# Kernel tuning notes

Measured on AMD Instinct MI355X. Metric: run time of the kernel, lower is better.

The kernel has to match this reference:

```python
import jax, jax.numpy as jnp
from jax import lax
import numpy as np

D_MODEL, N_STATES, N_GROUPS, K_CONV = 1024, 16, 8, 4
BATCH, LENGTH = 2, 2048


def setup_inputs() -> dict:
    key = jax.random.key(0)
    ks = jax.random.split(key, 8)
    x = jax.random.normal(ks[0], (BATCH, LENGTH, D_MODEL), dtype=jnp.float32)
    in_proj_w = jax.random.normal(ks[1], (2 * D_MODEL, D_MODEL), dtype=jnp.float32) * 0.02
    in_proj_b = jnp.zeros((2 * D_MODEL,), dtype=jnp.float32)
    delta_proj_w = jax.random.uniform(ks[2], (D_MODEL, D_MODEL), dtype=jnp.float32, minval=0.001, maxval=0.1)
    a_log = jnp.log(jnp.tile(jnp.arange(1, N_STATES + 1, dtype=jnp.float32), (D_MODEL, 1)))
    b_proj_w = jax.random.normal(ks[3], (N_GROUPS * N_STATES, D_MODEL), dtype=jnp.float32) * 1e-4
    b_proj_b = jnp.zeros((N_GROUPS * N_STATES,), dtype=jnp.float32)
    c_param = jax.random.normal(ks[4], (D_MODEL, N_STATES), dtype=jnp.float32) * 0.02
    # depthwise conv (groups = d_model): kernel [D, 1, K]
    conv_w = jax.random.normal(ks[5], (D_MODEL, 1, K_CONV), dtype=jnp.float32) * (1.0 / np.sqrt(K_CONV))
    conv_b = jnp.zeros((D_MODEL,), dtype=jnp.float32)
    return {"x": x, "in_proj_w": in_proj_w, "in_proj_b": in_proj_b,
            "delta_proj_w": delta_proj_w, "a_log": a_log,
            "b_proj_w": b_proj_w, "b_proj_b": b_proj_b, "c_param": c_param,
            "conv_w": conv_w, "conv_b": conv_b}


def _causal_conv(u, conv_w, conv_b):
    # u: [B, L, D] -> depthwise causal conv along L
    D = u.shape[-1]
    K = conv_w.shape[-1]
    uc = jnp.transpose(u, (0, 2, 1))  # [B, D, L]
    uc = lax.conv_general_dilated(uc, conv_w, window_strides=(1,),
                                  padding=[(K - 1, 0)], feature_group_count=D,
                                  dimension_numbers=("NCH", "OIH", "NCH"))
    uc = uc + conv_b[None, :, None]
    return jnp.transpose(uc, (0, 2, 1))  # [B, L, D]


def _selective_scan(delta, A, Bmat, c_param, u):
    # delta,u: [B,L,D]; A: [D,N]; Bmat: [B,L,G,N]; c_param: [D,N]
    Bsz, L, D = delta.shape
    N = A.shape[1]
    G = Bmat.shape[2]
    Bexp = jnp.repeat(Bmat, D // G, axis=2)            # [B,L,D,N]
    dA = jnp.exp(delta[..., None] * A)                  # [B,L,D,N]
    dBu = (delta * u)[..., None] * Bexp                 # [B,L,D,N]

    def step(h, xs):
        da, dbu = xs
        h = da * h + dbu                                # [B,D,N]
        y = jnp.einsum("bdn,dn->bd", h, c_param)
        return h, y

    h0 = jnp.zeros((Bsz, D, N), dtype=delta.dtype)
    _, ys = lax.scan(step, h0, (jnp.moveaxis(dA, 1, 0), jnp.moveaxis(dBu, 1, 0)))
    return jnp.moveaxis(ys, 0, 1)                       # [B,L,D]


def reference(x, in_proj_w, in_proj_b, delta_proj_w, a_log, b_proj_w, b_proj_b, c_param, conv_w, conv_b):
    Bsz, L, _ = x.shape
    N = a_log.shape[1]
    G = b_proj_w.shape[0] // N
    xp = x @ in_proj_w.T + in_proj_b                    # [B,L,2D]
    u, v = jnp.split(xp, 2, axis=-1)
    delta = jax.nn.softplus(u @ delta_proj_w.T)         # [B,L,D]
    A = -jnp.exp(a_log)                                 # [D,N]
    Bmat = (u @ b_proj_w.T + b_proj_b).reshape(Bsz, L, G, N)
    u_conv = jax.nn.silu(_causal_conv(u, conv_w, conv_b))
    y = _selective_scan(delta, A, Bmat, c_param, u_conv)
    return y * jax.nn.silu(v)
```

## Files before the change

kernel.cpp:

```cpp
#include <hip/hip_runtime.h>
#include <math.h>

#define LTOT 2048
#define MROWS 4096
#define CHK 64
#define NCH (LTOT / CHK)
#define SPAD 20

typedef short bf16x8 __attribute__((ext_vector_type(8)));
typedef float f32x4  __attribute__((ext_vector_type(4)));
typedef float f32x16 __attribute__((ext_vector_type(16)));

__device__ __forceinline__ unsigned short bf16_rne(float f) {
  unsigned u = __float_as_uint(f);
  u += 0x7FFF + ((u >> 16) & 1);
  return (unsigned short)(u >> 16);
}
__device__ __forceinline__ float bf16_to_f(unsigned short h) {
  return __uint_as_float(((unsigned)h) << 16);
}
__device__ __forceinline__ float softplus_f(float x) {
  return (x > 15.f) ? x : log1pf(expf(x));
}
__device__ __forceinline__ float silu_f(float x) {
  return x / (1.f + expf(-x));
}

__global__ void k_cvt_all(const float* __restrict__ x, const float* __restrict__ w1,
                          const float* __restrict__ dw, const float* __restrict__ bw,
                          unsigned short* __restrict__ xh, unsigned short* __restrict__ xl,
                          unsigned short* __restrict__ wfh, unsigned short* __restrict__ wfl,
                          unsigned short* __restrict__ wdbAh, unsigned short* __restrict__ wdbAl) {
  const int blk = blockIdx.x;
  const float* src; unsigned short *h, *l; int i;
  if (blk < 4096)      { src = x;  h = xh;  l = xl;  i = blk * 256 + threadIdx.x; }
  else if (blk < 6144) { src = w1; h = wfh; l = wfl; i = (blk - 4096) * 256 + threadIdx.x; }
  else if (blk < 7168) { src = dw; h = wdbAh; l = wdbAl; i = (blk - 6144) * 256 + threadIdx.x; }
  else                 { src = bw; h = wdbAh + (size_t)1024*1024; l = wdbAl + (size_t)1024*1024;
                         i = (blk - 7168) * 256 + threadIdx.x; }
  const float4 v = ((const float4*)src)[i];
  ushort4 hh, ll;
  hh.x = bf16_rne(v.x); ll.x = bf16_rne(v.x - bf16_to_f(hh.x));
  hh.y = bf16_rne(v.y); ll.y = bf16_rne(v.y - bf16_to_f(hh.y));
  hh.z = bf16_rne(v.z); ll.z = bf16_rne(v.z - bf16_to_f(hh.z));
  hh.w = bf16_rne(v.w); ll.w = bf16_rne(v.w - bf16_to_f(hh.w));
  ((ushort4*)h)[i] = hh;
  ((ushort4*)l)[i] = ll;
}

__global__ __launch_bounds__(256) void k_cvt_t(const float* __restrict__ w1,
    unsigned short* __restrict__ th, unsigned short* __restrict__ tl) {
  __shared__ float ts[64][65];
  const int t = threadIdx.x;
  const int j0 = blockIdx.y * 64, k0 = blockIdx.x * 64;
  const int r = t >> 4, c4 = (t & 15) * 4;
  #pragma unroll
  for (int p = 0; p < 4; ++p) {
    const int row = p * 16 + r;
    const float4 v = *(const float4*)&w1[(size_t)(j0 + row) * 1024 + k0 + c4];
    ts[row][c4] = v.x; ts[row][c4+1] = v.y; ts[row][c4+2] = v.z; ts[row][c4+3] = v.w;
  }
  __syncthreads();
  #pragma unroll
  for (int p = 0; p < 4; ++p) {
    const int rk = p * 16 + r;
    ushort4 hh, ll;
    float f;
    f = ts[c4+0][rk]; hh.x = bf16_rne(f); ll.x = bf16_rne(f - bf16_to_f(hh.x));
    f = ts[c4+1][rk]; hh.y = bf16_rne(f); ll.y = bf16_rne(f - bf16_to_f(hh.y));
    f = ts[c4+2][rk]; hh.z = bf16_rne(f); ll.z = bf16_rne(f - bf16_to_f(hh.z));
    f = ts[c4+3][rk]; hh.w = bf16_rne(f); ll.w = bf16_rne(f - bf16_to_f(hh.w));
    *(ushort4*)&th[(size_t)(k0 + rk) * 1024 + j0 + c4] = hh;
    *(ushort4*)&tl[(size_t)(k0 + rk) * 1024 + j0 + c4] = ll;
  }
}

__global__ void k_bias(const float* __restrict__ b1, const float* __restrict__ dw,
                       const float* __restrict__ bw, const float* __restrict__ bb,
                       float* __restrict__ bfull) {
  const int t = threadIdx.x;
  const int j = blockIdx.x * 16 + (t >> 4);
  const int lane16 = t & 15;
  const float* W = (j < 1024) ? (dw + (size_t)j * 1024) : (bw + (size_t)(j - 1024) * 1024);
  float s = 0.f;
  for (int i = 0; i < 64; ++i) {
    const int k = lane16 + i * 16;
    s = fmaf(b1[k], W[k], s);
  }
  s += __shfl_xor(s, 8, 16);
  s += __shfl_xor(s, 4, 16);
  s += __shfl_xor(s, 2, 16);
  s += __shfl_xor(s, 1, 16);
  if (lane16 == 0) bfull[j] = s + ((j >= 1024) ? bb[j - 1024] : 0.f);
}

__global__ __launch_bounds__(256) void k_wcomp(
    const unsigned short* __restrict__ Ah_g, const unsigned short* __restrict__ Al_g,
    const unsigned short* __restrict__ Bh_g, const unsigned short* __restrict__ Bl_g,
    unsigned short* __restrict__ outh, unsigned short* __restrict__ outl) {
  __shared__ __align__(16) unsigned short LAh[64*32];
  __shared__ __align__(16) unsigned short LAl[64*32];
  __shared__ __align__(16) unsigned short LBh[64*32];
  __shared__ __align__(16) unsigned short LBl[64*32];
  const int t = threadIdx.x;
  const int wave = t >> 6, lane = t & 63;
  const int m0 = blockIdx.y * 64, n0 = blockIdx.x * 64;
  const int wr = wave >> 1, wc = wave & 1;
  const int l32 = lane & 31, hi = lane >> 5;
  const int srow = lane >> 2, scol = (lane & 3) * 8;

  f32x16 acc;
  #pragma unroll
  for (int q = 0; q < 16; ++q) acc[q] = 0.f;

  auto stage = [&](const unsigned short* g, unsigned short* lds, int rbase, int k0) {
    const unsigned short* gp = g + (size_t)(rbase + wave * 16 + srow) * 1024 + k0 + scol;
    unsigned short* lp = lds + (wave * 16) * 32;
    __builtin_amdgcn_global_load_lds((const __attribute__((address_space(1))) void*)gp,
                                     (__attribute__((address_space(3))) void*)lp, 16, 0, 0);
  };

  for (int k0 = 0; k0 < 1024; k0 += 32) {
    __syncthreads();
    stage(Ah_g, LAh, m0, k0);
    stage(Al_g, LAl, m0, k0);
    stage(Bh_g, LBh, n0, k0);
    stage(Bl_g, LBl, n0, k0);
    __syncthreads();
    #pragma unroll
    for (int kh = 0; kh < 2; ++kh) {
      const int ai = (wr * 32 + l32) * 32 + kh * 16 + hi * 8;
      const int bi = (wc * 32 + l32) * 32 + kh * 16 + hi * 8;
      bf16x8 a_h = *(const bf16x8*)&LAh[ai];
      bf16x8 a_l = *(const bf16x8*)&LAl[ai];
      bf16x8 b_h = *(const bf16x8*)&LBh[bi];
      bf16x8 b_l = *(const bf16x8*)&LBl[bi];
      acc = __builtin_amdgcn_mfma_f32_32x32x16_bf16(a_h, b_h, acc, 0, 0, 0);
      acc = __builtin_amdgcn_mfma_f32_32x32x16_bf16(a_h, b_l, acc, 0, 0, 0);
      acc = __builtin_amdgcn_mfma_f32_32x32x16_bf16(a_l, b_h, acc, 0, 0, 0);
    }
  }

  #pragma unroll
  for (int reg = 0; reg < 16; ++reg) {
    const int i = m0 + wr * 32 + (reg & 3) + 8 * (reg >> 2) + 4 * hi;
    const int k = n0 + wc * 32 + l32;
    const float f = acc[reg];
    const unsigned short hh = bf16_rne(f);
    const unsigned short ll = bf16_rne(f - bf16_to_f(hh));
    outh[(size_t)i * 1024 + k] = hh;
    outl[(size_t)i * 1024 + k] = ll;
  }
}

__global__ __launch_bounds__(256) void k_main(
    const unsigned short* __restrict__ xh, const unsigned short* __restrict__ xl,
    const unsigned short* __restrict__ wfh, const unsigned short* __restrict__ wfl,
    const float* __restrict__ b1, const float* __restrict__ bfull,
    float* __restrict__ u_, float* __restrict__ v_,
    float* __restrict__ delta, float* __restrict__ Bm) {
  __shared__ __align__(16) unsigned short LAh[128*32];
  __shared__ __align__(16) unsigned short LAl[128*32];
  __shared__ __align__(16) unsigned short LBh[128*32];
  __shared__ __align__(16) unsigned short LBl[128*32];
  const int t = threadIdx.x;
  const int wave = t >> 6, lane = t & 63;
  const int flat = blockIdx.x;
  const int wg = (flat & 7) * 100 + (flat >> 3);
  const int tn = wg % 25;
  const int m0 = (wg / 25) * 128;
  const int wr = wave >> 1, wc = wave & 1;
  const int ln = lane & 15, kq = lane >> 4;
  const int srow = lane >> 2, scol = (lane & 3) * 8;
  const bool full = (tn >= 16);

  f32x4 acc[4][4];
  #pragma unroll
  for (int i = 0; i < 4; ++i)
    #pragma unroll
    for (int j = 0; j < 4; ++j) acc[i][j] = (f32x4){0.f, 0.f, 0.f, 0.f};

  const unsigned short* pAh = xh + (size_t)m0 * 1024;
  const unsigned short* pAl = xl + (size_t)m0 * 1024;
  const unsigned short* pBh = wfh + (size_t)(tn * 128) * 1024;
  const unsigned short* pBl = wfl + (size_t)(tn * 128) * 1024;

  auto stage = [&](const unsigned short* g, unsigned short* lds, int k0) {
    #pragma unroll
    for (int r = 0; r < 2; ++r) {
      const unsigned short* gp = g + (size_t)(r * 64 + wave * 16 + srow) * 1024 + k0 + scol;
      unsigned short* lp = lds + (r * 64 + wave * 16) * 32;
      __builtin_amdgcn_global_load_lds((const __attribute__((address_space(1))) void*)gp,
                                       (__attribute__((address_space(3))) void*)lp, 16, 0, 0);
    }
  };

  for (int k0 = 0; k0 < 1024; k0 += 32) {
    __syncthreads();
    stage(pAh, LAh, k0);
    stage(pBh, LBh, k0);
    if (full) { stage(pAl, LAl, k0); stage(pBl, LBl, k0); }
    __syncthreads();

    if (full) {
      bf16x8 ah[4], al[4], bh[4], bl[4];
      #pragma unroll
      for (int i = 0; i < 4; ++i) {
        const int ar = (wr * 64 + i * 16 + ln) * 32 + kq * 8;
        const int br = (wc * 64 + i * 16 + ln) * 32 + kq * 8;
        ah[i] = *(const bf16x8*)&LAh[ar];
        al[i] = *(const bf16x8*)&LAl[ar];
        bh[i] = *(const bf16x8*)&LBh[br];
        bl[i] = *(const bf16x8*)&LBl[br];
      }
      #pragma unroll
      for (int i = 0; i < 4; ++i)
        #pragma unroll
        for (int j = 0; j < 4; ++j) {
          acc[i][j] = __builtin_amdgcn_mfma_f32_16x16x32_bf16(ah[i], bh[j], acc[i][j], 0, 0, 0);
          acc[i][j] = __builtin_amdgcn_mfma_f32_16x16x32_bf16(ah[i], bl[j], acc[i][j], 0, 0, 0);
          acc[i][j] = __builtin_amdgcn_mfma_f32_16x16x32_bf16(al[i], bh[j], acc[i][j], 0, 0, 0);
        }
    } else {
      bf16x8 ah[4], bh[4];
      #pragma unroll
      for (int i = 0; i < 4; ++i) {
        const int ar = (wr * 64 + i * 16 + ln) * 32 + kq * 8;
        const int br = (wc * 64 + i * 16 + ln) * 32 + kq * 8;
        ah[i] = *(const bf16x8*)&LAh[ar];
        bh[i] = *(const bf16x8*)&LBh[br];
      }
      #pragma unroll
      for (int i = 0; i < 4; ++i)
        #pragma unroll
        for (int j = 0; j < 4; ++j)
          acc[i][j] = __builtin_amdgcn_mfma_f32_16x16x32_bf16(ah[i], bh[j], acc[i][j], 0, 0, 0);
    }
  }

  #pragma unroll
  for (int nj = 0; nj < 4; ++nj) {
    const int colg = tn * 128 + wc * 64 + nj * 16 + ln;
    const float bv = (tn < 16) ? b1[colg] : bfull[colg - 2048];
    #pragma unroll
    for (int mi = 0; mi < 4; ++mi) {
      const int row = m0 + wr * 64 + mi * 16 + kq * 4;
      #pragma unroll
      for (int j = 0; j < 4; ++j) {
        const float val = acc[mi][nj][j] + bv;
        if (tn < 8)       u_[(size_t)(row + j) * 1024 + colg] = val;
        else if (tn < 16) v_[(size_t)(row + j) * 1024 + colg - 1024] = val;
        else if (tn < 24) delta[(size_t)(row + j) * 1024 + colg - 2048] = softplus_f(val);
        else              Bm[(size_t)(row + j) * 128 + colg - 3072] = val;
      }
    }
  }
}

__global__ __launch_bounds__(256) void k_scanA(
    const float* __restrict__ delta, const float* __restrict__ u_,
    const float* __restrict__ Bm, const float* __restrict__ a_log,
    const float* __restrict__ cw, const float* __restrict__ cb,
    float* __restrict__ hend, float* __restrict__ Pp)
{
  __shared__ float sru[68][SPAD];
  __shared__ float sd[CHK][SPAD];
  __shared__ float sb[CHK][SPAD];
  __shared__ float suc[CHK][SPAD];
  const int t = threadIdx.x;
  const int bid = blockIdx.x;
  const int dblk = bid & 63;
  const int ch   = (bid >> 6) & (NCH - 1);
  const int b    = bid >> 11;
  const int d0 = dblk * 16;
  const int g  = dblk >> 3;
  const int l0 = ch * CHK;
  const size_t mb = (size_t)b * LTOT;

  {
    const int lrow = t >> 2;
    const int lc4  = (t & 3) * 4;
    const size_t r = mb + l0 + lrow;
    float4 rd = *(const float4*)&delta[r*1024 + d0 + lc4];
    float4 rb = *(const float4*)&Bm[r*128 + g*16 + lc4];
    *(float4*)&sd[lrow][lc4] = rd;
    *(float4*)&sb[lrow][lc4] = rb;
    const int sl = l0 + lrow - 4;
    float4 ru = (sl >= 0) ? *(const float4*)&u_[(mb + sl)*1024 + d0 + lc4]
                          : (float4){0.f, 0.f, 0.f, 0.f};
    *(float4*)&sru[lrow][lc4] = ru;
    if (t < 16) {
      const int rr2 = 64 + (t >> 2);
      const int sl2 = l0 + rr2 - 4;
      float4 r2 = *(const float4*)&u_[(mb + sl2)*1024 + d0 + (t & 3) * 4];
      *(float4*)&sru[rr2][(t & 3) * 4] = r2;
    }
  }
  __syncthreads();
  {
    const int c = t & 15;
    const int rb4 = (t >> 4) * 4;
    const float4 cwf = *(const float4*)&cw[(d0 + c) * 4];
    const float cbf = cb[d0 + c];
    #pragma unroll
    for (int q = 0; q < 4; ++q) {
      const int l = rb4 + q;
      float a = cbf;
      a = fmaf(sru[l+1][c], cwf.x, a);
      a = fmaf(sru[l+2][c], cwf.y, a);
      a = fmaf(sru[l+3][c], cwf.z, a);
      a = fmaf(sru[l+4][c], cwf.w, a);
      suc[l][c] = silu_f(a);
    }
  }
  __syncthreads();

  const int gi = t >> 4;
  const int n  = t & 15;
  const int d  = d0 + gi;
  const float A2 = -expf(a_log[d*16 + n]) * 1.4426950408889634f;

  float h = 0.f, P = 1.f;
  #pragma unroll 8
  for (int l = 0; l < CHK; ++l) {
    const float dv = sd[l][gi];
    const float uv = suc[l][gi];
    const float bv = sb[l][n];
    const float da = exp2f(dv * A2);
    P *= da;
    h = fmaf(da, h, dv * uv * bv);
  }
  const size_t idx = ((size_t)(b*NCH + ch) * 1024 + d) * 16 + n;
  hend[idx] = h;
  Pp[idx]   = P;
}

__global__ void k_scanB(float* hP, const float* __restrict__ Pp)
{
  const int t = blockIdx.x * 256 + threadIdx.x;
  const int b  = t >> 14;
  const int dn = t & 16383;
  float H = 0.f;
  for (int ch = 0; ch < NCH; ++ch) {
    const size_t idx = ((size_t)(b*NCH + ch) << 14) + dn;
    const float he = hP[idx];
    const float P  = Pp[idx];
    hP[idx] = H;
    H = fmaf(P, H, he);
  }
}

__global__ __launch_bounds__(256) void k_scanC(
    const float* __restrict__ v_, const float* __restrict__ delta,
    const float* __restrict__ u_, const float* __restrict__ Bm,
    const float* __restrict__ a_log, const float* __restrict__ cp,
    const float* __restrict__ cw, const float* __restrict__ cb,
    const float* __restrict__ Hstart, float* __restrict__ out)
{
  __shared__ float sru[68][SPAD];
  __shared__ float sd[CHK][SPAD];
  __shared__ float sb[CHK][SPAD];
  __shared__ float suc[CHK][SPAD];
  __shared__ float sv[CHK][SPAD];
  __shared__ float sy[CHK][SPAD];
  const int t = threadIdx.x;
  const int bid = blockIdx.x;
  const int dblk = bid & 63;
  const int ch   = (bid >> 6) & (NCH - 1);
  const int b    = bid >> 11;
  const int d0 = dblk * 16;
  const int g  = dblk >> 3;
  const int l0 = ch * CHK;
  const size_t mb = (size_t)b * LTOT;

  {
    const int lrow = t >> 2;
    const int lc4  = (t & 3) * 4;
    const size_t r = mb + l0 + lrow;
    float4 rd = *(const float4*)&delta[r*1024 + d0 + lc4];
    float4 rb = *(const float4*)&Bm[r*128 + g*16 + lc4];
    float4 rv = *(const float4*)&v_[r*1024 + d0 + lc4];
    *(float4*)&sd[lrow][lc4] = rd;
    *(float4*)&sb[lrow][lc4] = rb;
    *(float4*)&sv[lrow][lc4] = rv;
    const int sl = l0 + lrow - 4;
    float4 ru = (sl >= 0) ? *(const float4*)&u_[(mb + sl)*1024 + d0 + lc4]
                          : (float4){0.f, 0.f, 0.f, 0.f};
    *(float4*)&sru[lrow][lc4] = ru;
    if (t < 16) {
      const int rr2 = 64 + (t >> 2);
      const int sl2 = l0 + rr2 - 4;
      float4 r2 = *(const float4*)&u_[(mb + sl2)*1024 + d0 + (t & 3) * 4];
      *(float4*)&sru[rr2][(t & 3) * 4] = r2;
    }
  }
  __syncthreads();
  {
    const int c = t & 15;
    const int rb4 = (t >> 4) * 4;
    const float4 cwf = *(const float4*)&cw[(d0 + c) * 4];
    const float cbf = cb[d0 + c];
    #pragma unroll
    for (int q = 0; q < 4; ++q) {
      const int l = rb4 + q;
      float a = cbf;
      a = fmaf(sru[l+1][c], cwf.x, a);
      a = fmaf(sru[l+2][c], cwf.y, a);
      a = fmaf(sru[l+3][c], cwf.z, a);
      a = fmaf(sru[l+4][c], cwf.w, a);
      suc[l][c] = silu_f(a);
    }
  }
  __syncthreads();

  const int gi = t >> 4;
  const int n  = t & 15;
  const int d  = d0 + gi;
  const float A2 = -expf(a_log[d*16 + n]) * 1.4426950408889634f;
  const float cc = cp[d*16 + n];
  float h = Hstart[((size_t)(b*NCH + ch) * 1024 + d) * 16 + n];

  #pragma unroll
  for (int l16 = 0; l16 < CHK; l16 += 16) {
    float p[16];
    #pragma unroll
    for (int j = 0; j < 16; ++j) {
      const int l = l16 + j;
      const float dv = sd[l][gi];
      const float uv = suc[l][gi];
      const float bv = sb[l][n];
      const float da = exp2f(dv * A2);
      h = fmaf(da, h, dv * uv * bv);
      p[j] = h * cc;
    }
    float q8[8];
    #pragma unroll
    for (int j = 0; j < 8; ++j) {
      const float send = (n & 8) ? p[j]     : p[j + 8];
      const float keep = (n & 8) ? p[j + 8] : p[j];
      q8[j] = keep + __shfl_xor(send, 8, 16);
    }
    float q4[4];
    #pragma unroll
    for (int j = 0; j < 4; ++j) {
      const float send = (n & 4) ? q8[j]     : q8[j + 4];
      const float keep = (n & 4) ? q8[j + 4] : q8[j];
      q4[j] = keep + __shfl_xor(send, 4, 16);
    }
    float q2[2];
    #pragma unroll
    for (int j = 0; j < 2; ++j) {
      const float send = (n & 2) ? q4[j]     : q4[j + 2];
      const float keep = (n & 2) ? q4[j + 2] : q4[j];
      q2[j] = keep + __shfl_xor(send, 2, 16);
    }
    {
      const float send = (n & 1) ? q2[0] : q2[1];
      const float keep = (n & 1) ? q2[1] : q2[0];
      sy[l16 + n][gi] = keep + __shfl_xor(send, 1, 16);
    }
  }

  __syncthreads();
  const int rr = t >> 4;
  const int c  = t & 15;
  #pragma unroll
  for (int k = 0; k < 4; ++k) {
    const int r = rr + k * 16;
    const float vv = sv[r][c];
    out[(mb + l0 + r) * 1024 + d0 + c] = sy[r][c] * silu_f(vv);
  }
}

extern "C" void kernel_launch(void* const* d_in, const int* in_sizes, int n_in,
                              void* d_out, int out_size, void* d_ws, size_t ws_size,
                              hipStream_t stream) {
  const float* x    = (const float*)d_in[0];
  const float* w1   = (const float*)d_in[1];
  const float* b1   = (const float*)d_in[2];
  const float* dw   = (const float*)d_in[3];
  const float* alog = (const float*)d_in[4];
  const float* bw   = (const float*)d_in[5];
  const float* bb   = (const float*)d_in[6];
  const float* cp   = (const float*)d_in[7];
  const float* cw   = (const float*)d_in[8];
  const float* cb   = (const float*)d_in[9];
  float* out = (float*)d_out;

  const size_t M4 = (size_t)MROWS * 1024;
  float* u_    = (float*)d_ws;
  float* v_    = u_ + M4;
  float* delta = v_ + M4;
  float* Bm    = delta + M4;
  unsigned short* xh  = (unsigned short*)(Bm + (size_t)MROWS * 128);
  unsigned short* xl  = xh + M4;
  unsigned short* wfh = xl + M4;
  unsigned short* wfl = wfh + (size_t)3200 * 1024;
  float* bfull = (float*)(wfl + (size_t)3200 * 1024);
  unsigned short* wdbAh = (unsigned short*)delta;
  unsigned short* wdbAl = wdbAh + (size_t)1152 * 1024;
  unsigned short* w1th  = wdbAl + (size_t)1152 * 1024;
  unsigned short* w1tl  = w1th + (size_t)1024 * 1024;
  float* hend = (float*)wfh;
  float* Pp   = hend + (size_t)2 * NCH * 1024 * 16;

  k_cvt_all<<<7296, 256, 0, stream>>>(x, w1, dw, bw, xh, xl, wfh, wfl, wdbAh, wdbAl);
  k_cvt_t<<<dim3(16, 16), 256, 0, stream>>>(w1, w1th, w1tl);
  k_bias<<<72, 256, 0, stream>>>(b1, dw, bw, bb, bfull);
  k_wcomp<<<dim3(16, 18), 256, 0, stream>>>(wdbAh, wdbAl, w1th, w1tl,
                                            wfh + (size_t)2048*1024, wfl + (size_t)2048*1024);
  k_main<<<800, 256, 0, stream>>>(xh, xl, wfh, wfl, b1, bfull, u_, v_, delta, Bm);
  k_scanA<<<2 * NCH * 64, 256, 0, stream>>>(delta, u_, Bm, alog, cw, cb, hend, Pp);
  k_scanB<<<128, 256, 0, stream>>>(hend, Pp);
  k_scanC<<<2 * NCH * 64, 256, 0, stream>>>(v_, delta, u_, Bm, alog, cp, cw, cb, hend, out);
}
```

Before: 229.1 us.

## Split fused projection GEMM into uv/B and delta kernels, enlarge weight-compose tiles

The single mixed-precision projection kernel is split in two. One kernel computes u, v and the B projection with a single bf16 product. A separate kernel computes delta with the three-term hi/lo split-bf16 scheme, so no block carries a per-tile branch between cheap and expensive paths. The weight-composition GEMM moves to 128x128 tiles with 16x16 MFMAs and writes rows in a reordered layout, with B rows first and delta rows after. The trade-offs are an extra kernel launch, the loss of overlap between the uv and delta work, and reduced precision for the B projection, which drops its low-order terms.

After: 244.3 us. +6.7%, slower.

```diff
diff --git a/kernel.cpp b/kernel.cpp
--- a/kernel.cpp
+++ b/kernel.cpp
@@ -9,7 +9,6 @@
 
 typedef short bf16x8 __attribute__((ext_vector_type(8)));
 typedef float f32x4  __attribute__((ext_vector_type(4)));
-typedef float f32x16 __attribute__((ext_vector_type(16)));
 
 __device__ __forceinline__ unsigned short bf16_rne(float f) {
   unsigned u = __float_as_uint(f);
@@ -94,85 +93,21 @@
   if (lane16 == 0) bfull[j] = s + ((j >= 1024) ? bb[j - 1024] : 0.f);
 }
 
-__global__ __launch_bounds__(256) void k_wcomp(
+__global__ __launch_bounds__(256) void k_wcomp2(
     const unsigned short* __restrict__ Ah_g, const unsigned short* __restrict__ Al_g,
     const unsigned short* __restrict__ Bh_g, const unsigned short* __restrict__ Bl_g,
     unsigned short* __restrict__ outh, unsigned short* __restrict__ outl) {
-  __shared__ __align__(16) unsigned short LAh[64*32];
-  __shared__ __align__(16) unsigned short LAl[64*32];
-  __shared__ __align__(16) unsigned short LBh[64*32];
-  __shared__ __align__(16) unsigned short LBl[64*32];
-  const int t = threadIdx.x;
-  const int wave = t >> 6, lane = t & 63;
-  const int m0 = blockIdx.y * 64, n0 = blockIdx.x * 64;
-  const int wr = wave >> 1, wc = wave & 1;
-  const int l32 = lane & 31, hi = lane >> 5;
-  const int srow = lane >> 2, scol = (lane & 3) * 8;
-
-  f32x16 acc;
-  #pragma unroll
-  for (int q = 0; q < 16; ++q) acc[q] = 0.f;
-
-  auto stage = [&](const unsigned short* g, unsigned short* lds, int rbase, int k0) {
-    const unsigned short* gp = g + (size_t)(rbase + wave * 16 + srow) * 1024 + k0 + scol;
-    unsigned short* lp = lds + (wave * 16) * 32;
-    __builtin_amdgcn_global_load_lds((const __attribute__((address_space(1))) void*)gp,
-                                     (__attribute__((address_space(3))) void*)lp, 16, 0, 0);
-  };
-
-  for (int k0 = 0; k0 < 1024; k0 += 32) {
-    __syncthreads();
-    stage(Ah_g, LAh, m0, k0);
-    stage(Al_g, LAl, m0, k0);
-    stage(Bh_g, LBh, n0, k0);
-    stage(Bl_g, LBl, n0, k0);
-    __syncthreads();
-    #pragma unroll
-    for (int kh = 0; kh < 2; ++kh) {
-      const int ai = (wr * 32 + l32) * 32 + kh * 16 + hi * 8;
-      const int bi = (wc * 32 + l32) * 32 + kh * 16 + hi * 8;
-      bf16x8 a_h = *(const bf16x8*)&LAh[ai];
-      bf16x8 a_l = *(const bf16x8*)&LAl[ai];
-      bf16x8 b_h = *(const bf16x8*)&LBh[bi];
-      bf16x8 b_l = *(const bf16x8*)&LBl[bi];
-      acc = __builtin_amdgcn_mfma_f32_32x32x16_bf16(a_h, b_h, acc, 0, 0, 0);
-      acc = __builtin_amdgcn_mfma_f32_32x32x16_bf16(a_h, b_l, acc, 0, 0, 0);
-      acc = __builtin_amdgcn_mfma_f32_32x32x16_bf16(a_l, b_h, acc, 0, 0, 0);
-    }
-  }
-
-  #pragma unroll
-  for (int reg = 0; reg < 16; ++reg) {
-    const int i = m0 + wr * 32 + (reg & 3) + 8 * (reg >> 2) + 4 * hi;
-    const int k = n0 + wc * 32 + l32;
-    const float f = acc[reg];
-    const unsigned short hh = bf16_rne(f);
-    const unsigned short ll = bf16_rne(f - bf16_to_f(hh));
-    outh[(size_t)i * 1024 + k] = hh;
-    outl[(size_t)i * 1024 + k] = ll;
-  }
-}
-
-__global__ __launch_bounds__(256) void k_main(
-    const unsigned short* __restrict__ xh, const unsigned short* __restrict__ xl,
-    const unsigned short* __restrict__ wfh, const unsigned short* __restrict__ wfl,
-    const float* __restrict__ b1, const float* __restrict__ bfull,
-    float* __restrict__ u_, float* __restrict__ v_,
-    float* __restrict__ delta, float* __restrict__ Bm) {
   __shared__ __align__(16) unsigned short LAh[128*32];
   __shared__ __align__(16) unsigned short LAl[128*32];
   __shared__ __align__(16) unsigned short LBh[128*32];
   __shared__ __align__(16) unsigned short LBl[128*32];
   const int t = threadIdx.x;
   const int wave = t >> 6, lane = t & 63;
-  const int flat = blockIdx.x;
-  const int wg = (flat & 7) * 100 + (flat >> 3);
-  const int tn = wg % 25;
-  const int m0 = (wg / 25) * 128;
+  const int m0 = blockIdx.y * 128;
+  const int n0 = blockIdx.x * 128;
   const int wr = wave >> 1, wc = wave & 1;
   const int ln = lane & 15, kq = lane >> 4;
   const int srow = lane >> 2, scol = (lane & 3) * 8;
-  const bool full = (tn >= 16);
 
   f32x4 acc[4][4];
   #pragma unroll
@@ -180,10 +115,10 @@
     #pragma unroll
     for (int j = 0; j < 4; ++j) acc[i][j] = (f32x4){0.f, 0.f, 0.f, 0.f};
 
-  const unsigned short* pAh = xh + (size_t)m0 * 1024;
-  const unsigned short* pAl = xl + (size_t)m0 * 1024;
-  const unsigned short* pBh = wfh + (size_t)(tn * 128) * 1024;
-  const unsigned short* pBl = wfl + (size_t)(tn * 128) * 1024;
+  const unsigned short* pAh = Ah_g + (size_t)m0 * 1024;
+  const unsigned short* pAl = Al_g + (size_t)m0 * 1024;
+  const unsigned short* pBh = Bh_g + (size_t)n0 * 1024;
+  const unsigned short* pBl = Bl_g + (size_t)n0 * 1024;
 
   auto stage = [&](const unsigned short* g, unsigned short* lds, int k0) {
     #pragma unroll
@@ -198,50 +133,108 @@
   for (int k0 = 0; k0 < 1024; k0 += 32) {
     __syncthreads();
     stage(pAh, LAh, k0);
+    stage(pAl, LAl, k0);
     stage(pBh, LBh, k0);
-    if (full) { stage(pAl, LAl, k0); stage(pBl, LBl, k0); }
+    stage(pBl, LBl, k0);
     __syncthreads();
-
-    if (full) {
-      bf16x8 ah[4], al[4], bh[4], bl[4];
+    bf16x8 ah[4], al[4], bh[4], bl[4];
+    #pragma unroll
+    for (int i = 0; i < 4; ++i) {
+      const int ar = (wr * 64 + i * 16 + ln) * 32 + kq * 8;
+      const int br = (wc * 64 + i * 16 + ln) * 32 + kq * 8;
+      ah[i] = *(const bf16x8*)&LAh[ar];
+      al[i] = *(const bf16x8*)&LAl[ar];
+      bh[i] = *(const bf16x8*)&LBh[br];
+      bl[i] = *(const bf16x8*)&LBl[br];
+    }
+    #pragma unroll
+    for (int i = 0; i < 4; ++i)
       #pragma unroll
-      for (int i = 0; i < 4; ++i) {
-        const int ar = (wr * 64 + i * 16 + ln) * 32 + kq * 8;
-        const int br = (wc * 64 + i * 16 + ln) * 32 + kq * 8;
-        ah[i] = *(const bf16x8*)&LAh[ar];
-        al[i] = *(const bf16x8*)&LAl[ar];
-        bh[i] = *(const bf16x8*)&LBh[br];
-        bl[i] = *(const bf16x8*)&LBl[br];
+      for (int j = 0; j < 4; ++j) {
+        acc[i][j] = __builtin_amdgcn_mfma_f32_16x16x32_bf16(ah[i], bh[j], acc[i][j], 0, 0, 0);
+        acc[i][j] = __builtin_amdgcn_mfma_f32_16x16x32_bf16(ah[i], bl[j], acc[i][j], 0, 0, 0);
+        acc[i][j] = __builtin_amdgcn_mfma_f32_16x16x32_bf16(al[i], bh[j], acc[i][j], 0, 0, 0);
       }
+  }
+
+  const int rbase = (blockIdx.y < 8) ? 2176 : 1024;
+  #pragma unroll
+  for (int nj = 0; nj < 4; ++nj) {
+    const int kcol = n0 + wc * 64 + nj * 16 + ln;
+    #pragma unroll
+    for (int mi = 0; mi < 4; ++mi) {
+      const int i = m0 + wr * 64 + mi * 16 + kq * 4;
       #pragma unroll
-      for (int i = 0; i < 4; ++i)
-        #pragma unroll
-        for (int j = 0; j < 4; ++j) {
-          acc[i][j] = __builtin_amdgcn_mfma_f32_16x16x32_bf16(ah[i], bh[j], acc[i][j], 0, 0, 0);
-          acc[i][j] = __builtin_amdgcn_mfma_f32_16x16x32_bf16(ah[i], bl[j], acc[i][j], 0, 0, 0);
-          acc[i][j] = __builtin_amdgcn_mfma_f32_16x16x32_bf16(al[i], bh[j], acc[i][j], 0, 0, 0);
-        }
-    } else {
-      bf16x8 ah[4], bh[4];
+      for (int j = 0; j < 4; ++j) {
+        const float f = acc[mi][nj][j];
+        const unsigned short hh = bf16_rne(f);
+        const unsigned short ll = bf16_rne(f - bf16_to_f(hh));
+        outh[(size_t)(rbase + i + j) * 1024 + kcol] = hh;
+        outl[(size_t)(rbase + i + j) * 1024 + kcol] = ll;
+      }
+    }
+  }
+}
+
+__global__ __launch_bounds__(256) void k_uv(
+    const unsigned short* __restrict__ xh, const unsigned short* __restrict__ wfh,
+    const float* __restrict__ b1, const float* __restrict__ bfull,
+    float* __restrict__ u_, float* __restrict__ v_, float* __restrict__ Bm) {
+  __shared__ __align__(16) unsigned short LAh[128*32];
+  __shared__ __align__(16) unsigned short LBh[128*32];
+  const int t = threadIdx.x;
+  const int wave = t >> 6, lane = t & 63;
+  const int flat = blockIdx.x;
+  const int wg = (flat & 7) * 68 + (flat >> 3);
+  const int tn = wg % 17;
+  const int m0 = (wg / 17) * 128;
+  const int wr = wave >> 1, wc = wave & 1;
+  const int ln = lane & 15, kq = lane >> 4;
+  const int srow = lane >> 2, scol = (lane & 3) * 8;
+
+  f32x4 acc[4][4];
+  #pragma unroll
+  for (int i = 0; i < 4; ++i)
+    #pragma unroll
+    for (int j = 0; j < 4; ++j) acc[i][j] = (f32x4){0.f, 0.f, 0.f, 0.f};
+
+  const unsigned short* pAh = xh + (size_t)m0 * 1024;
+  const unsigned short* pBh = wfh + (size_t)(tn * 128) * 1024;
+
+  auto stage = [&](const unsigned short* g, unsigned short* lds, int k0) {
+    #pragma unroll
+    for (int r = 0; r < 2; ++r) {
+      const unsigned short* gp = g + (size_t)(r * 64 + wave * 16 + srow) * 1024 + k0 + scol;
+      unsigned short* lp = lds + (r * 64 + wave * 16) * 32;
+      __builtin_amdgcn_global_load_lds((const __attribute__((address_space(1))) void*)gp,
+                                       (__attribute__((address_space(3))) void*)lp, 16, 0, 0);
+    }
+  };
+
+  for (int k0 = 0; k0 < 1024; k0 += 32) {
+    __syncthreads();
+    stage(pAh, LAh, k0);
+    stage(pBh, LBh, k0);
+    __syncthreads();
+    bf16x8 ah[4], bh[4];
+    #pragma unroll
+    for (int i = 0; i < 4; ++i) {
+      const int ar = (wr * 64 + i * 16 + ln) * 32 + kq * 8;
+      const int br = (wc * 64 + i * 16 + ln) * 32 + kq * 8;
+      ah[i] = *(const bf16x8*)&LAh[ar];
+      bh[i] = *(const bf16x8*)&LBh[br];
+    }
+    #pragma unroll
+    for (int i = 0; i < 4; ++i)
       #pragma unroll
-      for (int i = 0; i < 4; ++i) {
-        const int ar = (wr * 64 + i * 16 + ln) * 32 + kq * 8;
-        const int br = (wc * 64 + i * 16 + ln) * 32 + kq * 8;
-        ah[i] = *(const bf16x8*)&LAh[ar];
-        bh[i] = *(const bf16x8*)&LBh[br];
-      }
-      #pragma unroll
-      for (int i = 0; i < 4; ++i)
-        #pragma unroll
-        for (int j = 0; j < 4; ++j)
-          acc[i][j] = __builtin_amdgcn_mfma_f32_16x16x32_bf16(ah[i], bh[j], acc[i][j], 0, 0, 0);
-    }
+      for (int j = 0; j < 4; ++j)
+        acc[i][j] = __builtin_amdgcn_mfma_f32_16x16x32_bf16(ah[i], bh[j], acc[i][j], 0, 0, 0);
   }
 
   #pragma unroll
   for (int nj = 0; nj < 4; ++nj) {
     const int colg = tn * 128 + wc * 64 + nj * 16 + ln;
-    const float bv = (tn < 16) ? b1[colg] : bfull[colg - 2048];
+    const float bv = (tn < 16) ? b1[colg] : bfull[1024 + colg - 2048];
     #pragma unroll
     for (int mi = 0; mi < 4; ++mi) {
       const int row = m0 + wr * 64 + mi * 16 + kq * 4;
@@ -250,9 +243,88 @@
         const float val = acc[mi][nj][j] + bv;
         if (tn < 8)       u_[(size_t)(row + j) * 1024 + colg] = val;
         else if (tn < 16) v_[(size_t)(row + j) * 1024 + colg - 1024] = val;
-        else if (tn < 24) delta[(size_t)(row + j) * 1024 + colg - 2048] = softplus_f(val);
-        else              Bm[(size_t)(row + j) * 128 + colg - 3072] = val;
+        else              Bm[(size_t)(row + j) * 128 + colg - 2048] = val;
       }
+    }
+  }
+}
+
+__global__ __launch_bounds__(256) void k_d(
+    const unsigned short* __restrict__ xh, const unsigned short* __restrict__ xl,
+    const unsigned short* __restrict__ wfh, const unsigned short* __restrict__ wfl,
+    const float* __restrict__ bfull, float* __restrict__ delta) {
+  __shared__ __align__(16) unsigned short LAh[128*32];
+  __shared__ __align__(16) unsigned short LAl[128*32];
+  __shared__ __align__(16) unsigned short LBh[128*32];
+  __shared__ __align__(16) unsigned short LBl[128*32];
+  const int t = threadIdx.x;
+  const int wave = t >> 6, lane = t & 63;
+  const int flat = blockIdx.x;
+  const int wg = (flat & 7) * 32 + (flat >> 3);
+  const int tn = wg & 7;
+  const int m0 = (wg >> 3) * 128;
+  const int wr = wave >> 1, wc = wave & 1;
+  const int ln = lane & 15, kq = lane >> 4;
+  const int srow = lane >> 2, scol = (lane & 3) * 8;
+
+  f32x4 acc[4][4];
+  #pragma unroll
+  for (int i = 0; i < 4; ++i)
+    #pragma unroll
+    for (int j = 0; j < 4; ++j) acc[i][j] = (f32x4){0.f, 0.f, 0.f, 0.f};
+
+  const unsigned short* pAh = xh + (size_t)m0 * 1024;
+  const unsigned short* pAl = xl + (size_t)m0 * 1024;
+  const unsigned short* pBh = wfh + (size_t)(2176 + tn * 128) * 1024;
+  const unsigned short* pBl = wfl + (size_t)(2176 + tn * 128) * 1024;
+
+  auto stage = [&](const unsigned short* g, unsigned short* lds, int k0) {
+    #pragma unroll
+    for (int r = 0; r < 2; ++r) {
+      const unsigned short* gp = g + (size_t)(r * 64 + wave * 16 + srow) * 1024 + k0 + scol;
+      unsigned short* lp = lds + (r * 64 + wave * 16) * 32;
+      __builtin_amdgcn_global_load_lds((const __attribute__((address_space(1))) void*)gp,
+                                       (__attribute__((address_space(3))) void*)lp, 16, 0, 0);
+    }
+  };
+
+  for (int k0 = 0; k0 < 1024; k0 += 32) {
+    __syncthreads();
+    stage(pAh, LAh, k0);
+    stage(pAl, LAl, k0);
+    stage(pBh, LBh, k0);
+    stage(pBl, LBl, k0);
+    __syncthreads();
+    bf16x8 ah[4], al[4], bh[4], bl[4];
+    #pragma unroll
+    for (int i = 0; i < 4; ++i) {
+      const int ar = (wr * 64 + i * 16 + ln) * 32 + kq * 8;
+      const int br = (wc * 64 + i * 16 + ln) * 32 + kq * 8;
+      ah[i] = *(const bf16x8*)&LAh[ar];
+      al[i] = *(const bf16x8*)&LAl[ar];
+      bh[i] = *(const bf16x8*)&LBh[br];
+      bl[i] = *(const bf16x8*)&LBl[br];
+    }
+    #pragma unroll
+    for (int i = 0; i < 4; ++i)
+      #pragma unroll
+      for (int j = 0; j < 4; ++j) {
+        acc[i][j] = __builtin_amdgcn_mfma_f32_16x16x32_bf16(ah[i], bh[j], acc[i][j], 0, 0, 0);
+        acc[i][j] = __builtin_amdgcn_mfma_f32_16x16x32_bf16(ah[i], bl[j], acc[i][j], 0, 0, 0);
+        acc[i][j] = __builtin_amdgcn_mfma_f32_16x16x32_bf16(al[i], bh[j], acc[i][j], 0, 0, 0);
+      }
+  }
+
+  #pragma unroll
+  for (int nj = 0; nj < 4; ++nj) {
+    const int colg = tn * 128 + wc * 64 + nj * 16 + ln;
+    const float bv = bfull[colg];
+    #pragma unroll
+    for (int mi = 0; mi < 4; ++mi) {
+      const int row = m0 + wr * 64 + mi * 16 + kq * 4;
+      #pragma unroll
+      for (int j = 0; j < 4; ++j)
+        delta[(size_t)(row + j) * 1024 + colg] = softplus_f(acc[mi][nj][j] + bv);
     }
   }
 }
@@ -507,9 +579,9 @@
   k_cvt_all<<<7296, 256, 0, stream>>>(x, w1, dw, bw, xh, xl, wfh, wfl, wdbAh, wdbAl);
   k_cvt_t<<<dim3(16, 16), 256, 0, stream>>>(w1, w1th, w1tl);
   k_bias<<<72, 256, 0, stream>>>(b1, dw, bw, bb, bfull);
-  k_wcomp<<<dim3(16, 18), 256, 0, stream>>>(wdbAh, wdbAl, w1th, w1tl,
-                                            wfh + (size_t)2048*1024, wfl + (size_t)2048*1024);
-  k_main<<<800, 256, 0, stream>>>(xh, xl, wfh, wfl, b1, bfull, u_, v_, delta, Bm);
+  k_wcomp2<<<dim3(8, 9), 256, 0, stream>>>(wdbAh, wdbAl, w1th, w1tl, wfh, wfl);
+  k_uv<<<544, 256, 0, stream>>>(xh, wfh, b1, bfull, u_, v_, Bm);
+  k_d<<<256, 256, 0, stream>>>(xh, xl, wfh, wfl, bfull, delta);
   k_scanA<<<2 * NCH * 64, 256, 0, stream>>>(delta, u_, Bm, alog, cw, cb, hend, Pp);
   k_scanB<<<128, 256, 0, stream>>>(hend, Pp);
   k_scanC<<<2 * NCH * 64, 256, 0, stream>>>(v_, delta, u_, Bm, alog, cp, cw, cb, hend, out);
```
